# Kernel optimization log

Measured on AMD Instinct MI355X. Metric: run time of the kernel, lower is better.

The kernel has to match this reference:

```python
import jax, jax.numpy as jnp
import numpy as np

S, N, K, B = 4, 16384, 128, 131072  # num_sim, nodes, k_dim, num pairs


def setup_inputs() -> dict:
    key = jax.random.key(0)
    ks = jax.random.split(key, 16)
    sc = 0.05
    return {
        "X": jax.random.normal(ks[0], (S, N, K), jnp.float32),
        "Y": jax.random.normal(ks[1], (S, N, K), jnp.float32),
        "x_att": jax.random.normal(ks[2], (S,), jnp.float32),
        "y_att": jax.random.normal(ks[3], (S,), jnp.float32),
        "W_cX1": jax.random.normal(ks[4], (S * K, 1), jnp.float32) * sc,
        "b_cX1": jnp.zeros((1,), jnp.float32),
        "W_cX2": jax.random.normal(ks[5], (1, K), jnp.float32) * sc,
        "b_cX2": jnp.zeros((K,), jnp.float32),
        "W_cY1": jax.random.normal(ks[6], (S * K, 1), jnp.float32) * sc,
        "b_cY1": jnp.zeros((1,), jnp.float32),
        "W_cY2": jax.random.normal(ks[7], (1, K), jnp.float32) * sc,
        "b_cY2": jnp.zeros((K,), jnp.float32),
        "W0": jax.random.normal(ks[8], (2 * K, K), jnp.float32) * sc,
        "b0": jnp.zeros((K,), jnp.float32),
        "W1": jax.random.normal(ks[9], (K, K // 2), jnp.float32) * sc,
        "b1": jnp.zeros((K // 2,), jnp.float32),
        "W2": jax.random.normal(ks[10], (K // 2, 1), jnp.float32) * sc,
        "b2": jnp.zeros((1,), jnp.float32),
        "idx0": jax.random.randint(ks[11], (B,), 0, N, jnp.int32),
        "idx1": jax.random.randint(ks[12], (B,), 0, N, jnp.int32),
    }


def _embed(Z, idx, att_vec, Wc1, bc1, Wc2, bc2):
    """0.5 * (sim_5 + sim_8) embedding for one side. Z: [S,N,K], idx: [B]."""
    lrelu = jax.nn.leaky_relu  # negative_slope=0.01, matches torch default
    Zs = jnp.transpose(Z[:, idx, :], (1, 0, 2))            # [B, S, K]
    Zsum = Zs.sum(axis=1)                                   # [B, K]
    # sim_5: concat views -> scalar -> K attention, softmax over K
    Zcat = Zs.reshape(Zs.shape[0], -1)                      # [B, S*K]
    att = jax.nn.softmax(lrelu(Zcat @ Wc1 + bc1) @ Wc2 + bc2, axis=-1)
    e5 = Zsum * att                                         # [B, K]
    # sim_8: softmax-weighted sum over views
    e8 = jnp.einsum('bsk,s->bk', Zs, jax.nn.softmax(att_vec))
    return 0.5 * (e5 + e8)


def reference(X, Y, x_att, y_att,
              W_cX1, b_cX1, W_cX2, b_cX2,
              W_cY1, b_cY1, W_cY2, b_cY2,
              W0, b0, W1, b1, W2, b2,
              idx0, idx1):
    lrelu = jax.nn.leaky_relu
    X_embed = _embed(X, idx0, x_att, W_cX1, b_cX1, W_cX2, b_cX2)  # [B, K]
    Y_embed = _embed(Y, idx1, y_att, W_cY1, b_cY1, W_cY2, b_cY2)  # [B, K]
    # get_pred, score_type='cat': decoder0 -> decoder1 -> decoder2 -> sigmoid
    feat = jnp.concatenate([X_embed, Y_embed], axis=1)             # [B, 2K]
    o = lrelu(feat @ W0 + b0)                                      # [B, K]
    o = lrelu(o @ W1 + b1)                                         # [B, K/2]
    pred = (o @ W2 + b2).ravel()                                   # [B]
    return jax.nn.sigmoid(pred)
```

## Files before the change

### kernel.cpp

```cpp
#include <hip/hip_runtime.h>
#include <hip/hip_bf16.h>

#define S_   4
#define N_   16384
#define K_   128

typedef __attribute__((ext_vector_type(8))) short short8v;
typedef __attribute__((ext_vector_type(4))) float f32x4;

__device__ __forceinline__ float lrelu(float x) { return x > 0.f ? x : 0.01f * x; }

__device__ __forceinline__ unsigned short f2bf(float f) {
    union { float f; unsigned u; } v; v.f = f;
    unsigned r = v.u + 0x7fff + ((v.u >> 16) & 1);
    return (unsigned short)(r >> 16);
}

__global__ __launch_bounds__(256)
void convert_w(const float* __restrict__ W0, const float* __restrict__ W1,
               unsigned short* __restrict__ W0T, unsigned short* __restrict__ W1T)
{
    int t = blockIdx.x * 256 + threadIdx.x;
    if (t < 128 * 256) {
        int n = t >> 8, k = t & 255;
        W0T[t] = f2bf(W0[k * 128 + n]);
    }
    t -= 128 * 256;
    if (t >= 0 && t < 64 * 128) {
        int n = t >> 7, k = t & 127;
        W1T[t] = f2bf(W1[k * 64 + n]);
    }
}

__global__ __launch_bounds__(256)
void node_embed(const float* __restrict__ X, const float* __restrict__ Y,
                const float* __restrict__ x_att, const float* __restrict__ y_att,
                const float* __restrict__ WcX1, const float* __restrict__ bcX1,
                const float* __restrict__ WcX2, const float* __restrict__ bcX2,
                const float* __restrict__ WcY1, const float* __restrict__ bcY1,
                const float* __restrict__ WcY2, const float* __restrict__ bcY2,
                unsigned short* __restrict__ Xemb, unsigned short* __restrict__ Yemb)
{
    const int node = blockIdx.x * 4 + (threadIdx.x >> 6);
    if (node >= N_) return;
    const int lane = threadIdx.x & 63;
    const int half = lane >> 5;
    const int sl   = lane & 31;
    const int k0   = sl * 4;

    const float* Z    = half ? Y    : X;
    const float* Wc1  = half ? WcY1 : WcX1;
    const float* Wc2  = half ? WcY2 : WcX2;
    const float* bc2h = half ? bcY2 : bcX2;
    const float  bc1v = half ? bcY1[0] : bcX1[0];
    const float* attv = half ? y_att : x_att;
    unsigned short* dst = half ? Yemb : Xemb;

    float a0 = attv[0], a1 = attv[1], a2 = attv[2], a3 = attv[3];
    float am = fmaxf(fmaxf(a0, a1), fmaxf(a2, a3));
    float sw0 = __expf(a0 - am), sw1 = __expf(a1 - am),
          sw2 = __expf(a2 - am), sw3 = __expf(a3 - am);
    float swinv = 1.f / (sw0 + sw1 + sw2 + sw3);
    sw0 *= swinv; sw1 *= swinv; sw2 *= swinv; sw3 *= swinv;

    float4 z0 = *(const float4*)(Z + ((size_t)0 * N_ + node) * K_ + k0);
    float4 z1 = *(const float4*)(Z + ((size_t)1 * N_ + node) * K_ + k0);
    float4 z2 = *(const float4*)(Z + ((size_t)2 * N_ + node) * K_ + k0);
    float4 z3 = *(const float4*)(Z + ((size_t)3 * N_ + node) * K_ + k0);

    float4 zs;
    zs.x = z0.x + z1.x + z2.x + z3.x;
    zs.y = z0.y + z1.y + z2.y + z3.y;
    zs.z = z0.z + z1.z + z2.z + z3.z;
    zs.w = z0.w + z1.w + z2.w + z3.w;

    float4 w0 = *(const float4*)(Wc1 + 0 * K_ + k0);
    float4 w1 = *(const float4*)(Wc1 + 1 * K_ + k0);
    float4 w2 = *(const float4*)(Wc1 + 2 * K_ + k0);
    float4 w3 = *(const float4*)(Wc1 + 3 * K_ + k0);
    float dp = z0.x*w0.x + z0.y*w0.y + z0.z*w0.z + z0.w*w0.w
             + z1.x*w1.x + z1.y*w1.y + z1.z*w1.z + z1.w*w1.w
             + z2.x*w2.x + z2.y*w2.y + z2.z*w2.z + z2.w*w2.w
             + z3.x*w3.x + z3.y*w3.y + z3.z*w3.z + z3.w*w3.w;
#pragma unroll
    for (int off = 16; off >= 1; off >>= 1) dp += __shfl_xor(dp, off, 64);

    float a = lrelu(dp + bc1v);

    float4 c2 = *(const float4*)(Wc2 + k0);
    float4 cb = *(const float4*)(bc2h + k0);
    float l0 = fmaf(a, c2.x, cb.x), l1 = fmaf(a, c2.y, cb.y);
    float l2 = fmaf(a, c2.z, cb.z), l3 = fmaf(a, c2.w, cb.w);
    float m = fmaxf(fmaxf(l0, l1), fmaxf(l2, l3));
#pragma unroll
    for (int off = 16; off >= 1; off >>= 1) m = fmaxf(m, __shfl_xor(m, off, 64));
    float e0 = __expf(l0 - m), e1 = __expf(l1 - m),
          e2 = __expf(l2 - m), e3 = __expf(l3 - m);
    float s = e0 + e1 + e2 + e3;
#pragma unroll
    for (int off = 16; off >= 1; off >>= 1) s += __shfl_xor(s, off, 64);
    float inv = 1.f / s;

    float o0v = 0.5f * (zs.x * (e0 * inv) + (sw0*z0.x + sw1*z1.x + sw2*z2.x + sw3*z3.x));
    float o1v = 0.5f * (zs.y * (e1 * inv) + (sw0*z0.y + sw1*z1.y + sw2*z2.y + sw3*z3.y));
    float o2v = 0.5f * (zs.z * (e2 * inv) + (sw0*z0.z + sw1*z1.z + sw2*z2.z + sw3*z3.z));
    float o3v = 0.5f * (zs.w * (e3 * inv) + (sw0*z0.w + sw1*z1.w + sw2*z2.w + sw3*z3.w));

    ushort4 p;
    p.x = f2bf(o0v); p.y = f2bf(o1v); p.z = f2bf(o2v); p.w = f2bf(o3v);
    *(ushort4*)(dst + (size_t)node * K_ + k0) = p;
}

__global__ __launch_bounds__(256)
void decoder_kernel(const unsigned short* __restrict__ Xemb,
                    const unsigned short* __restrict__ Yemb,
                    const unsigned short* __restrict__ W0T,
                    const unsigned short* __restrict__ W1T,
                    const float* __restrict__ b0, const float* __restrict__ b1,
                    const float* __restrict__ W2, const float* __restrict__ b2,
                    const int* __restrict__ idx0, const int* __restrict__ idx1,
                    float* __restrict__ out, int Btot)
{
    __shared__ unsigned short o0[128 * 136];

    const int wave = threadIdx.x >> 6;
    const int lane = threadIdx.x & 63;
    const int lx   = lane & 15;
    const int lk   = lane >> 4;
    const int rowBase = blockIdx.x * 128 + wave * 32;

    int r0 = rowBase + lx;       if (r0 >= Btot) r0 = Btot - 1;
    int r1 = rowBase + 16 + lx;  if (r1 >= Btot) r1 = Btot - 1;
    const unsigned short* xb0 = Xemb + (size_t)idx0[r0] * K_;
    const unsigned short* xb1 = Xemb + (size_t)idx0[r1] * K_;
    const unsigned short* yb0 = Yemb + (size_t)idx1[r0] * K_;
    const unsigned short* yb1 = Yemb + (size_t)idx1[r1] * K_;

    f32x4 acc[2][8];
#pragma unroll
    for (int m = 0; m < 2; ++m)
#pragma unroll
        for (int n = 0; n < 8; ++n) acc[m][n] = (f32x4)0.f;

#pragma unroll
    for (int kk = 0; kk < 8; ++kk) {
        const int koff = kk * 32 + lk * 8;
        short8v a0, a1;
        if (kk < 4) {
            a0 = *(const short8v*)(xb0 + koff);
            a1 = *(const short8v*)(xb1 + koff);
        } else {
            a0 = *(const short8v*)(yb0 + koff - 128);
            a1 = *(const short8v*)(yb1 + koff - 128);
        }
#pragma unroll
        for (int n = 0; n < 8; ++n) {
            short8v b = *(const short8v*)(W0T + (size_t)(n * 16 + lx) * 256 + koff);
            acc[0][n] = __builtin_amdgcn_mfma_f32_16x16x32_bf16(a0, b, acc[0][n], 0, 0, 0);
            acc[1][n] = __builtin_amdgcn_mfma_f32_16x16x32_bf16(a1, b, acc[1][n], 0, 0, 0);
        }
    }

    {
        float b0v[8];
#pragma unroll
        for (int n = 0; n < 8; ++n) b0v[n] = b0[n * 16 + lx];
#pragma unroll
        for (int m = 0; m < 2; ++m)
#pragma unroll
            for (int n = 0; n < 8; ++n)
#pragma unroll
                for (int r = 0; r < 4; ++r) {
                    float v = lrelu(acc[m][n][r] + b0v[n]);
                    int row = wave * 32 + m * 16 + lk * 4 + r;
                    o0[row * 136 + n * 16 + lx] = f2bf(v);
                }
    }

    f32x4 acc1[2][4];
#pragma unroll
    for (int m = 0; m < 2; ++m)
#pragma unroll
        for (int n = 0; n < 4; ++n) acc1[m][n] = (f32x4)0.f;

#pragma unroll
    for (int kk = 0; kk < 4; ++kk) {
        const int koff = kk * 32 + lk * 8;
        short8v a0 = *(const short8v*)(&o0[(wave * 32 + lx) * 136 + koff]);
        short8v a1 = *(const short8v*)(&o0[(wave * 32 + 16 + lx) * 136 + koff]);
#pragma unroll
        for (int n = 0; n < 4; ++n) {
            short8v b = *(const short8v*)(W1T + (size_t)(n * 16 + lx) * 128 + koff);
            acc1[0][n] = __builtin_amdgcn_mfma_f32_16x16x32_bf16(a0, b, acc1[0][n], 0, 0, 0);
            acc1[1][n] = __builtin_amdgcn_mfma_f32_16x16x32_bf16(a1, b, acc1[1][n], 0, 0, 0);
        }
    }

    {
        float w2v[4], b1v[4];
#pragma unroll
        for (int n = 0; n < 4; ++n) {
            w2v[n] = W2[n * 16 + lx];
            b1v[n] = b1[n * 16 + lx];
        }
        const float b2v = b2[0];
        float t[2][4];
#pragma unroll
        for (int m = 0; m < 2; ++m)
#pragma unroll
            for (int r = 0; r < 4; ++r) t[m][r] = 0.f;
#pragma unroll
        for (int m = 0; m < 2; ++m)
#pragma unroll
            for (int n = 0; n < 4; ++n)
#pragma unroll
                for (int r = 0; r < 4; ++r) {
                    float v = lrelu(acc1[m][n][r] + b1v[n]);
                    t[m][r] = fmaf(v, w2v[n], t[m][r]);
                }
#pragma unroll
        for (int off = 8; off >= 1; off >>= 1)
#pragma unroll
            for (int m = 0; m < 2; ++m)
#pragma unroll
                for (int r = 0; r < 4; ++r)
                    t[m][r] += __shfl_xor(t[m][r], off, 64);
        if (lx == 0) {
#pragma unroll
            for (int m = 0; m < 2; ++m)
#pragma unroll
                for (int r = 0; r < 4; ++r) {
                    int row = rowBase + m * 16 + lk * 4 + r;
                    if (row < Btot)
                        out[row] = 1.f / (1.f + __expf(-(t[m][r] + b2v)));
                }
        }
    }
}

#define PPB  32
#define NT   256
#define FSTR 260
#define O0STR 132
#define O1STR 68

__device__ __forceinline__ void embed_side_f(
    const float* __restrict__ Z, int idx,
    const float* __restrict__ Wc1, float bc1v,
    const float* __restrict__ Wc2, const float* __restrict__ bc2,
    float sw0, float sw1, float sw2, float sw3,
    int lane, float* dst)
{
    const int k0 = 2 * lane;
    const float* base = Z + (size_t)idx * K_ + k0;
    float2 z0 = *(const float2*)(base + (size_t)0 * N_ * K_);
    float2 z1 = *(const float2*)(base + (size_t)1 * N_ * K_);
    float2 z2 = *(const float2*)(base + (size_t)2 * N_ * K_);
    float2 z3 = *(const float2*)(base + (size_t)3 * N_ * K_);
    float zs0 = z0.x + z1.x + z2.x + z3.x;
    float zs1 = z0.y + z1.y + z2.y + z3.y;
    float2 w0 = *(const float2*)(Wc1 + 0 * K_ + k0);
    float2 w1 = *(const float2*)(Wc1 + 1 * K_ + k0);
    float2 w2 = *(const float2*)(Wc1 + 2 * K_ + k0);
    float2 w3 = *(const float2*)(Wc1 + 3 * K_ + k0);
    float dp = z0.x*w0.x + z0.y*w0.y + z1.x*w1.x + z1.y*w1.y
             + z2.x*w2.x + z2.y*w2.y + z3.x*w3.x + z3.y*w3.y;
#pragma unroll
    for (int off = 32; off >= 1; off >>= 1) dp += __shfl_xor(dp, off, 64);
    float a = lrelu(dp + bc1v);
    float2 c2 = *(const float2*)(Wc2 + k0);
    float2 cb = *(const float2*)(bc2 + k0);
    float l0 = fmaf(a, c2.x, cb.x), l1 = fmaf(a, c2.y, cb.y);
    float m = fmaxf(l0, l1);
#pragma unroll
    for (int off = 32; off >= 1; off >>= 1) m = fmaxf(m, __shfl_xor(m, off, 64));
    float e0 = __expf(l0 - m), e1 = __expf(l1 - m);
    float s = e0 + e1;
#pragma unroll
    for (int off = 32; off >= 1; off >>= 1) s += __shfl_xor(s, off, 64);
    float inv = 1.f / s;
    float e8a = sw0*z0.x + sw1*z1.x + sw2*z2.x + sw3*z3.x;
    float e8b = sw0*z0.y + sw1*z1.y + sw2*z2.y + sw3*z3.y;
    *(float2*)(dst + k0) = make_float2(0.5f*(zs0*(e0*inv)+e8a), 0.5f*(zs1*(e1*inv)+e8b));
}

__global__ __launch_bounds__(NT)
void mf_fused(const float* __restrict__ X, const float* __restrict__ Y,
              const float* __restrict__ x_att, const float* __restrict__ y_att,
              const float* __restrict__ WcX1, const float* __restrict__ bcX1,
              const float* __restrict__ WcX2, const float* __restrict__ bcX2,
              const float* __restrict__ WcY1, const float* __restrict__ bcY1,
              const float* __restrict__ WcY2, const float* __restrict__ bcY2,
              const float* __restrict__ W0, const float* __restrict__ b0,
              const float* __restrict__ W1, const float* __restrict__ b1,
              const float* __restrict__ W2, const float* __restrict__ b2,
              const int* __restrict__ idx0, const int* __restrict__ idx1,
              float* __restrict__ out, int Btot)
{
    __shared__ float pool[PPB * FSTR];
    float* feat = pool;
    const int tid  = threadIdx.x;
    const int lane = tid & 63;
    const int wave = tid >> 6;
    float swx0, swx1, swx2, swx3, swy0, swy1, swy2, swy3;
    {
        float a0 = x_att[0], a1 = x_att[1], a2 = x_att[2], a3 = x_att[3];
        float m = fmaxf(fmaxf(a0, a1), fmaxf(a2, a3));
        float e0 = __expf(a0-m), e1 = __expf(a1-m), e2 = __expf(a2-m), e3 = __expf(a3-m);
        float inv = 1.f / (e0+e1+e2+e3);
        swx0=e0*inv; swx1=e1*inv; swx2=e2*inv; swx3=e3*inv;
        float b0v=y_att[0], b1v=y_att[1], b2v=y_att[2], b3v=y_att[3];
        float my = fmaxf(fmaxf(b0v,b1v), fmaxf(b2v,b3v));
        float f0=__expf(b0v-my), f1=__expf(b1v-my), f2=__expf(b2v-my), f3=__expf(b3v-my);
        float invy = 1.f/(f0+f1+f2+f3);
        swy0=f0*invy; swy1=f1*invy; swy2=f2*invy; swy3=f3*invy;
    }
    const float bcX1v = bcX1[0], bcY1v = bcY1[0];
    const long pair_base = (long)blockIdx.x * PPB;
    for (int pp = 0; pp < PPB/4; ++pp) {
        const int p_local = wave * (PPB/4) + pp;
        const long pair = pair_base + p_local;
        if (pair < Btot) {
            embed_side_f(X, idx0[pair], WcX1, bcX1v, WcX2, bcX2, swx0,swx1,swx2,swx3, lane, feat + p_local*FSTR);
            embed_side_f(Y, idx1[pair], WcY1, bcY1v, WcY2, bcY2, swy0,swy1,swy2,swy3, lane, feat + p_local*FSTR + K_);
        }
    }
    __syncthreads();
    const int jg = tid & 15, pg = tid >> 4;
    float acc[2][8];
#pragma unroll
    for (int p=0;p<2;++p)
#pragma unroll
        for (int j=0;j<8;++j) acc[p][j]=0.f;
    const float* frow0 = feat + (pg*2+0)*FSTR;
    const float* frow1 = feat + (pg*2+1)*FSTR;
    for (int i = 0; i < 2*K_; i += 4) {
        float fav[4], fbv[4];
        *(float4*)fav = *(const float4*)(frow0+i);
        *(float4*)fbv = *(const float4*)(frow1+i);
#pragma unroll
        for (int u=0;u<4;++u) {
            float wv[8];
            *(float4*)(wv)   = *(const float4*)(W0 + (i+u)*K_ + jg*8);
            *(float4*)(wv+4) = *(const float4*)(W0 + (i+u)*K_ + jg*8 + 4);
#pragma unroll
            for (int j=0;j<8;++j) {
                acc[0][j] = fmaf(fav[u], wv[j], acc[0][j]);
                acc[1][j] = fmaf(fbv[u], wv[j], acc[1][j]);
            }
        }
    }
    __syncthreads();
    float* o0 = pool;
    {
        float bv[8];
        *(float4*)bv     = *(const float4*)(b0 + jg*8);
        *(float4*)(bv+4) = *(const float4*)(b0 + jg*8 + 4);
#pragma unroll
        for (int p=0;p<2;++p) {
            float v[8];
#pragma unroll
            for (int j=0;j<8;++j) v[j] = lrelu(acc[p][j] + bv[j]);
            *(float4*)(o0 + (pg*2+p)*O0STR + jg*8)     = *(float4*)v;
            *(float4*)(o0 + (pg*2+p)*O0STR + jg*8 + 4) = *(float4*)(v+4);
        }
    }
    __syncthreads();
    float acc1[2][4];
#pragma unroll
    for (int p=0;p<2;++p)
#pragma unroll
        for (int j=0;j<4;++j) acc1[p][j]=0.f;
    const float* r0 = o0 + (pg*2+0)*O0STR;
    const float* r1 = o0 + (pg*2+1)*O0STR;
    for (int i = 0; i < K_; i += 4) {
        float fav[4], fbv[4];
        *(float4*)fav = *(const float4*)(r0+i);
        *(float4*)fbv = *(const float4*)(r1+i);
#pragma unroll
        for (int u=0;u<4;++u) {
            float wv[4];
            *(float4*)wv = *(const float4*)(W1 + (i+u)*(K_/2) + jg*4);
#pragma unroll
            for (int j=0;j<4;++j) {
                acc1[0][j] = fmaf(fav[u], wv[j], acc1[0][j]);
                acc1[1][j] = fmaf(fbv[u], wv[j], acc1[1][j]);
            }
        }
    }
    float* o1 = pool + PPB*O0STR;
    {
        float bv[4];
        *(float4*)bv = *(const float4*)(b1 + jg*4);
#pragma unroll
        for (int p=0;p<2;++p) {
            float v[4];
#pragma unroll
            for (int j=0;j<4;++j) v[j] = lrelu(acc1[p][j] + bv[j]);
            *(float4*)(o1 + (pg*2+p)*O1STR + jg*4) = *(float4*)v;
        }
    }
    __syncthreads();
    {
        const int p = tid >> 3, part = tid & 7;
        const float* r = o1 + p*O1STR + part*8;
        float rv[8], wv[8];
        *(float4*)rv     = *(const float4*)(r);
        *(float4*)(rv+4) = *(const float4*)(r+4);
        *(float4*)wv     = *(const float4*)(W2 + part*8);
        *(float4*)(wv+4) = *(const float4*)(W2 + part*8 + 4);
        float d = 0.f;
#pragma unroll
        for (int j=0;j<8;++j) d = fmaf(rv[j], wv[j], d);
        d += __shfl_xor(d, 1, 64);
        d += __shfl_xor(d, 2, 64);
        d += __shfl_xor(d, 4, 64);
        if (part == 0) {
            const long pair = pair_base + p;
            if (pair < Btot) out[pair] = 1.f / (1.f + __expf(-(d + b2[0])));
        }
    }
}

extern "C" void kernel_launch(void* const* d_in, const int* in_sizes, int n_in,
                              void* d_out, int out_size, void* d_ws, size_t ws_size,
                              hipStream_t stream) {
    const float* X    = (const float*)d_in[0];
    const float* Y    = (const float*)d_in[1];
    const float* xatt = (const float*)d_in[2];
    const float* yatt = (const float*)d_in[3];
    const float* WcX1 = (const float*)d_in[4];
    const float* bcX1 = (const float*)d_in[5];
    const float* WcX2 = (const float*)d_in[6];
    const float* bcX2 = (const float*)d_in[7];
    const float* WcY1 = (const float*)d_in[8];
    const float* bcY1 = (const float*)d_in[9];
    const float* WcY2 = (const float*)d_in[10];
    const float* bcY2 = (const float*)d_in[11];
    const float* W0   = (const float*)d_in[12];
    const float* b0   = (const float*)d_in[13];
    const float* W1   = (const float*)d_in[14];
    const float* b1   = (const float*)d_in[15];
    const float* W2   = (const float*)d_in[16];
    const float* b2   = (const float*)d_in[17];
    const int* idx0   = (const int*)d_in[18];
    const int* idx1   = (const int*)d_in[19];
    float* out        = (float*)d_out;

    const int Btot = in_sizes[18];
    const int dblocks = (Btot + 127) / 128;
    const size_t need = (9u << 20);

    if (ws_size >= need) {
        unsigned short* W0T  = (unsigned short*)d_ws;
        unsigned short* W1T  = (unsigned short*)((char*)d_ws + 65536);
        unsigned short* Xemb = (unsigned short*)((char*)d_ws + (1u << 20));
        unsigned short* Yemb = (unsigned short*)((char*)d_ws + (5u << 20));

        convert_w<<<(128*256 + 64*128 + 255) / 256, 256, 0, stream>>>(W0, W1, W0T, W1T);
        node_embed<<<N_ / 4, 256, 0, stream>>>(
            X, Y, xatt, yatt, WcX1, bcX1, WcX2, bcX2,
            WcY1, bcY1, WcY2, bcY2, Xemb, Yemb);
        decoder_kernel<<<dblocks, 256, 0, stream>>>(
            Xemb, Yemb, W0T, W1T, b0, b1, W2, b2, idx0, idx1, out, Btot);
    } else {
        mf_fused<<<(Btot + PPB - 1) / PPB, NT, 0, stream>>>(
            X, Y, xatt, yatt, WcX1, bcX1, WcX2, bcX2,
            WcY1, bcY1, WcY2, bcY2, W0, b0, W1, b1, W2, b2,
            idx0, idx1, out, Btot);
    }
}
```

Before: 196.6 us.

## Merge weight conversion into node-embed kernel and prefetch decoder operands

The weight transpose/bf16 conversion kernel is folded into the node embedding kernel as extra leading blocks, removing one kernel launch. In the decoder, all A-fragments from the gathered embeddings and the bias/W2 values are loaded up front. B fragments are loaded in batches per k-step, and launch bounds request 4 blocks per CU. This aims to hide gather latency and launch overhead, at the cost of higher register pressure that could spill under the occupancy hint.

```diff
diff --git a/kernel.cpp b/kernel.cpp
--- a/kernel.cpp
+++ b/kernel.cpp
@@ -4,6 +4,7 @@
 #define S_   4
 #define N_   16384
 #define K_   128
+#define CONV_BLOCKS 160
 
 typedef __attribute__((ext_vector_type(8))) short short8v;
 typedef __attribute__((ext_vector_type(4))) float f32x4;
@@ -17,31 +18,31 @@
 }
 
 __global__ __launch_bounds__(256)
-void convert_w(const float* __restrict__ W0, const float* __restrict__ W1,
-               unsigned short* __restrict__ W0T, unsigned short* __restrict__ W1T)
+void embed_convert(const float* __restrict__ X, const float* __restrict__ Y,
+                   const float* __restrict__ x_att, const float* __restrict__ y_att,
+                   const float* __restrict__ WcX1, const float* __restrict__ bcX1,
+                   const float* __restrict__ WcX2, const float* __restrict__ bcX2,
+                   const float* __restrict__ WcY1, const float* __restrict__ bcY1,
+                   const float* __restrict__ WcY2, const float* __restrict__ bcY2,
+                   const float* __restrict__ W0, const float* __restrict__ W1,
+                   unsigned short* __restrict__ W0T, unsigned short* __restrict__ W1T,
+                   unsigned short* __restrict__ Xemb, unsigned short* __restrict__ Yemb)
 {
-    int t = blockIdx.x * 256 + threadIdx.x;
-    if (t < 128 * 256) {
-        int n = t >> 8, k = t & 255;
-        W0T[t] = f2bf(W0[k * 128 + n]);
-    }
-    t -= 128 * 256;
-    if (t >= 0 && t < 64 * 128) {
-        int n = t >> 7, k = t & 127;
-        W1T[t] = f2bf(W1[k * 64 + n]);
-    }
-}
-
-__global__ __launch_bounds__(256)
-void node_embed(const float* __restrict__ X, const float* __restrict__ Y,
-                const float* __restrict__ x_att, const float* __restrict__ y_att,
-                const float* __restrict__ WcX1, const float* __restrict__ bcX1,
-                const float* __restrict__ WcX2, const float* __restrict__ bcX2,
-                const float* __restrict__ WcY1, const float* __restrict__ bcY1,
-                const float* __restrict__ WcY2, const float* __restrict__ bcY2,
-                unsigned short* __restrict__ Xemb, unsigned short* __restrict__ Yemb)
-{
-    const int node = blockIdx.x * 4 + (threadIdx.x >> 6);
+    if (blockIdx.x < CONV_BLOCKS) {
+        int t = blockIdx.x * 256 + threadIdx.x;
+        if (t < 128 * 256) {
+            int n = t >> 8, k = t & 255;
+            W0T[t] = f2bf(W0[k * 128 + n]);
+        }
+        t -= 128 * 256;
+        if (t >= 0 && t < 64 * 128) {
+            int n = t >> 7, k = t & 127;
+            W1T[t] = f2bf(W1[k * 64 + n]);
+        }
+        return;
+    }
+
+    const int node = (blockIdx.x - CONV_BLOCKS) * 4 + (threadIdx.x >> 6);
     if (node >= N_) return;
     const int lane = threadIdx.x & 63;
     const int half = lane >> 5;
@@ -67,6 +68,12 @@
     float4 z1 = *(const float4*)(Z + ((size_t)1 * N_ + node) * K_ + k0);
     float4 z2 = *(const float4*)(Z + ((size_t)2 * N_ + node) * K_ + k0);
     float4 z3 = *(const float4*)(Z + ((size_t)3 * N_ + node) * K_ + k0);
+    float4 w0 = *(const float4*)(Wc1 + 0 * K_ + k0);
+    float4 w1 = *(const float4*)(Wc1 + 1 * K_ + k0);
+    float4 w2 = *(const float4*)(Wc1 + 2 * K_ + k0);
+    float4 w3 = *(const float4*)(Wc1 + 3 * K_ + k0);
+    float4 c2 = *(const float4*)(Wc2 + k0);
+    float4 cb = *(const float4*)(bc2h + k0);
 
     float4 zs;
     zs.x = z0.x + z1.x + z2.x + z3.x;
@@ -74,10 +81,6 @@
     zs.z = z0.z + z1.z + z2.z + z3.z;
     zs.w = z0.w + z1.w + z2.w + z3.w;
 
-    float4 w0 = *(const float4*)(Wc1 + 0 * K_ + k0);
-    float4 w1 = *(const float4*)(Wc1 + 1 * K_ + k0);
-    float4 w2 = *(const float4*)(Wc1 + 2 * K_ + k0);
-    float4 w3 = *(const float4*)(Wc1 + 3 * K_ + k0);
     float dp = z0.x*w0.x + z0.y*w0.y + z0.z*w0.z + z0.w*w0.w
              + z1.x*w1.x + z1.y*w1.y + z1.z*w1.z + z1.w*w1.w
              + z2.x*w2.x + z2.y*w2.y + z2.z*w2.z + z2.w*w2.w
@@ -87,8 +90,6 @@
 
     float a = lrelu(dp + bc1v);
 
-    float4 c2 = *(const float4*)(Wc2 + k0);
-    float4 cb = *(const float4*)(bc2h + k0);
     float l0 = fmaf(a, c2.x, cb.x), l1 = fmaf(a, c2.y, cb.y);
     float l2 = fmaf(a, c2.z, cb.z), l3 = fmaf(a, c2.w, cb.w);
     float m = fmaxf(fmaxf(l0, l1), fmaxf(l2, l3));
@@ -111,7 +112,7 @@
     *(ushort4*)(dst + (size_t)node * K_ + k0) = p;
 }
 
-__global__ __launch_bounds__(256)
+__global__ __launch_bounds__(256, 4)
 void decoder_kernel(const unsigned short* __restrict__ Xemb,
                     const unsigned short* __restrict__ Yemb,
                     const unsigned short* __restrict__ W0T,
@@ -131,10 +132,26 @@
 
     int r0 = rowBase + lx;       if (r0 >= Btot) r0 = Btot - 1;
     int r1 = rowBase + 16 + lx;  if (r1 >= Btot) r1 = Btot - 1;
-    const unsigned short* xb0 = Xemb + (size_t)idx0[r0] * K_;
-    const unsigned short* xb1 = Xemb + (size_t)idx0[r1] * K_;
-    const unsigned short* yb0 = Yemb + (size_t)idx1[r0] * K_;
-    const unsigned short* yb1 = Yemb + (size_t)idx1[r1] * K_;
+    const unsigned short* xb0 = Xemb + (size_t)idx0[r0] * K_ + lk * 8;
+    const unsigned short* xb1 = Xemb + (size_t)idx0[r1] * K_ + lk * 8;
+    const unsigned short* yb0 = Yemb + (size_t)idx1[r0] * K_ + lk * 8;
+    const unsigned short* yb1 = Yemb + (size_t)idx1[r1] * K_ + lk * 8;
+
+    float b0v[8], b1v[4], w2v[4];
+#pragma unroll
+    for (int n = 0; n < 8; ++n) b0v[n] = b0[n * 16 + lx];
+#pragma unroll
+    for (int n = 0; n < 4; ++n) { b1v[n] = b1[n * 16 + lx]; w2v[n] = W2[n * 16 + lx]; }
+    const float b2v = b2[0];
+
+    short8v A0[8], A1[8];
+#pragma unroll
+    for (int kk = 0; kk < 4; ++kk) {
+        A0[kk]     = *(const short8v*)(xb0 + kk * 32);
+        A1[kk]     = *(const short8v*)(xb1 + kk * 32);
+        A0[kk + 4] = *(const short8v*)(yb0 + kk * 32);
+        A1[kk + 4] = *(const short8v*)(yb1 + kk * 32);
+    }
 
     f32x4 acc[2][8];
 #pragma unroll
@@ -145,65 +162,57 @@
 #pragma unroll
     for (int kk = 0; kk < 8; ++kk) {
         const int koff = kk * 32 + lk * 8;
-        short8v a0, a1;
-        if (kk < 4) {
-            a0 = *(const short8v*)(xb0 + koff);
-            a1 = *(const short8v*)(xb1 + koff);
-        } else {
-            a0 = *(const short8v*)(yb0 + koff - 128);
-            a1 = *(const short8v*)(yb1 + koff - 128);
-        }
+        short8v Bv[8];
+#pragma unroll
+        for (int n = 0; n < 8; ++n)
+            Bv[n] = *(const short8v*)(W0T + (size_t)(n * 16 + lx) * 256 + koff);
 #pragma unroll
         for (int n = 0; n < 8; ++n) {
-            short8v b = *(const short8v*)(W0T + (size_t)(n * 16 + lx) * 256 + koff);
-            acc[0][n] = __builtin_amdgcn_mfma_f32_16x16x32_bf16(a0, b, acc[0][n], 0, 0, 0);
-            acc[1][n] = __builtin_amdgcn_mfma_f32_16x16x32_bf16(a1, b, acc[1][n], 0, 0, 0);
-        }
-    }
-
-    {
-        float b0v[8];
-#pragma unroll
-        for (int n = 0; n < 8; ++n) b0v[n] = b0[n * 16 + lx];
-#pragma unroll
-        for (int m = 0; m < 2; ++m)
-#pragma unroll
-            for (int n = 0; n < 8; ++n)
-#pragma unroll
-                for (int r = 0; r < 4; ++r) {
-                    float v = lrelu(acc[m][n][r] + b0v[n]);
-                    int row = wave * 32 + m * 16 + lk * 4 + r;
-                    o0[row * 136 + n * 16 + lx] = f2bf(v);
-                }
-    }
-
-    f32x4 acc1[2][4];
+            acc[0][n] = __builtin_amdgcn_mfma_f32_16x16x32_bf16(A0[kk], Bv[n], acc[0][n], 0, 0, 0);
+            acc[1][n] = __builtin_amdgcn_mfma_f32_16x16x32_bf16(A1[kk], Bv[n], acc[1][n], 0, 0, 0);
+        }
+    }
+
 #pragma unroll
     for (int m = 0; m < 2; ++m)
 #pragma unroll
-        for (int n = 0; n < 4; ++n) acc1[m][n] = (f32x4)0.f;
-
+        for (int n = 0; n < 8; ++n)
+#pragma unroll
+            for (int r = 0; r < 4; ++r) {
+                float v = lrelu(acc[m][n][r] + b0v[n]);
+                int row = wave * 32 + m * 16 + lk * 4 + r;
+                o0[row * 136 + n * 16 + lx] = f2bf(v);
+            }
+
+    short8v La0[4], La1[4];
 #pragma unroll
     for (int kk = 0; kk < 4; ++kk) {
         const int koff = kk * 32 + lk * 8;
-        short8v a0 = *(const short8v*)(&o0[(wave * 32 + lx) * 136 + koff]);
-        short8v a1 = *(const short8v*)(&o0[(wave * 32 + 16 + lx) * 136 + koff]);
+        La0[kk] = *(const short8v*)(&o0[(wave * 32 + lx) * 136 + koff]);
+        La1[kk] = *(const short8v*)(&o0[(wave * 32 + 16 + lx) * 136 + koff]);
+    }
+
+    f32x4 acc1[2][4];
+#pragma unroll
+    for (int m = 0; m < 2; ++m)
+#pragma unroll
+        for (int n = 0; n < 4; ++n) acc1[m][n] = (f32x4)0.f;
+
+#pragma unroll
+    for (int kk = 0; kk < 4; ++kk) {
+        const int koff = kk * 32 + lk * 8;
+        short8v Bv1[4];
+#pragma unroll
+        for (int n = 0; n < 4; ++n)
+            Bv1[n] = *(const short8v*)(W1T + (size_t)(n * 16 + lx) * 128 + koff);
 #pragma unroll
         for (int n = 0; n < 4; ++n) {
-            short8v b = *(const short8v*)(W1T + (size_t)(n * 16 + lx) * 128 + koff);
-            acc1[0][n] = __builtin_amdgcn_mfma_f32_16x16x32_bf16(a0, b, acc1[0][n], 0, 0, 0);
-            acc1[1][n] = __builtin_amdgcn_mfma_f32_16x16x32_bf16(a1, b, acc1[1][n], 0, 0, 0);
+            acc1[0][n] = __builtin_amdgcn_mfma_f32_16x16x32_bf16(La0[kk], Bv1[n], acc1[0][n], 0, 0, 0);
+            acc1[1][n] = __builtin_amdgcn_mfma_f32_16x16x32_bf16(La1[kk], Bv1[n], acc1[1][n], 0, 0, 0);
         }
     }
 
     {
-        float w2v[4], b1v[4];
-#pragma unroll
-        for (int n = 0; n < 4; ++n) {
-            w2v[n] = W2[n * 16 + lx];
-            b1v[n] = b1[n * 16 + lx];
-        }
-        const float b2v = b2[0];
         float t[2][4];
 #pragma unroll
         for (int m = 0; m < 2; ++m)
@@ -457,10 +466,9 @@
         unsigned short* Xemb = (unsigned short*)((char*)d_ws + (1u << 20));
         unsigned short* Yemb = (unsigned short*)((char*)d_ws + (5u << 20));
 
-        convert_w<<<(128*256 + 64*128 + 255) / 256, 256, 0, stream>>>(W0, W1, W0T, W1T);
-        node_embed<<<N_ / 4, 256, 0, stream>>>(
+        embed_convert<<<CONV_BLOCKS + N_ / 4, 256, 0, stream>>>(
             X, Y, xatt, yatt, WcX1, bcX1, WcX2, bcX2,
-            WcY1, bcY1, WcY2, bcY2, Xemb, Yemb);
+            WcY1, bcY1, WcY2, bcY2, W0, W1, W0T, W1T, Xemb, Yemb);
         decoder_kernel<<<dblocks, 256, 0, stream>>>(
             Xemb, Yemb, W0T, W1T, b0, b1, W2, b2, idx0, idx1, out, Btot);
     } else {
```

New measurement: 180.5 us. -8.2%, faster.
